# Optimization experiments

Measured on AMD Instinct MI355X. Metric: run time of the kernel, lower is better.

The kernel has to match this reference:

```python
import jax, jax.numpy as jnp
import numpy as np

EMB = 1024
HEADS = 16


def setup_inputs() -> dict:
    key = jax.random.key(0)
    ks = jax.random.split(key, 5)
    s = 1.0 / np.sqrt(EMB).astype(np.float32)
    return {
        "x": jax.random.normal(ks[0], (4, 2048, EMB), dtype=jnp.float32),
        "Wq": jax.random.normal(ks[1], (EMB, EMB), dtype=jnp.float32) * s,
        "bq": jnp.zeros((EMB,), dtype=jnp.float32),
        "Wk": jax.random.normal(ks[2], (EMB, EMB), dtype=jnp.float32) * s,
        "bk": jnp.zeros((EMB,), dtype=jnp.float32),
        "Wv": jax.random.normal(ks[3], (EMB, EMB), dtype=jnp.float32) * s,
        "bv": jnp.zeros((EMB,), dtype=jnp.float32),
        "Wo": jax.random.normal(ks[4], (EMB, EMB), dtype=jnp.float32) * s,
        "bo": jnp.zeros((EMB,), dtype=jnp.float32),
    }


def reference(x, Wq, bq, Wk, bk, Wv, bv, Wo, bo):
    b, n, e = x.shape
    h = HEADS
    d = e // h
    # QKV projections, split heads: [b, n, e] -> [b, h, n, d]
    def split_heads(t):
        return t.reshape(b, n, h, d).transpose(0, 2, 1, 3)
    q = split_heads(x @ Wq + bq)
    k = split_heads(x @ Wk + bk)
    v = split_heads(x @ Wv + bv)
    # NOTE: original scales by sqrt(emb_size), not sqrt(head_dim)
    energy = jnp.einsum('bhqd,bhkd->bhqk', q, k)
    att = jax.nn.softmax(energy / jnp.sqrt(jnp.float32(e)), axis=-1)
    # dropout is identity in eval mode
    out = jnp.einsum('bhqk,bhkd->bhqd', att, v)
    out = out.transpose(0, 2, 1, 3).reshape(b, n, e)
    return out @ Wo + bo
```

## Files before the change

### kernel.cpp

```cpp
#include <hip/hip_runtime.h>

#define EMB   1024
#define SEQ   2048
#define BATCH 4
#define HEADS 16
#define HDIM  64
#define MTOT  8192

typedef __bf16 bf16x8 __attribute__((ext_vector_type(8)));
typedef float  fx4    __attribute__((ext_vector_type(4)));

#if __has_builtin(__builtin_amdgcn_exp2f)
#define EXP2(x) __builtin_amdgcn_exp2f(x)
#else
#define EXP2(x) exp2f(x)
#endif

__device__ __forceinline__ unsigned short f2bf(float f) {
    unsigned u = __builtin_bit_cast(unsigned, f);
    u += 0x7fffu + ((u >> 16) & 1u);
    return (unsigned short)(u >> 16);
}
__device__ __forceinline__ unsigned short bfbits(float f) {
    __bf16 h = (__bf16)f;
    return __builtin_bit_cast(unsigned short, h);
}

#define AS1 __attribute__((address_space(1)))
#define AS3 __attribute__((address_space(3)))
__device__ __forceinline__ void glds16(const void* g, void* l) {
    __builtin_amdgcn_global_load_lds((AS1 void*)g, (AS3 void*)l, 16, 0, 0);
}
#define DRAIN_GLDS() __builtin_amdgcn_s_waitcnt(0x0f70)

#define QSCALE 0.0450842137604569f

__global__ __launch_bounds__(256) void cvt_x_kernel(const float* __restrict__ x,
                                                    unsigned short* __restrict__ xb)
{
    const int idx = (blockIdx.x * 256 + threadIdx.x) * 4;
    const float4 v = *(const float4*)(x + idx);
    ushort4 o;
    o.x = f2bf(v.x); o.y = f2bf(v.y); o.z = f2bf(v.z); o.w = f2bf(v.w);
    *(ushort4*)(xb + idx) = o;
}

__global__ __launch_bounds__(256) void cvt_w_kernel(
    const float* __restrict__ w0, const float* __restrict__ w1,
    const float* __restrict__ w2, const float* __restrict__ w3,
    unsigned short* __restrict__ o0, unsigned short* __restrict__ o1,
    unsigned short* __restrict__ o2, unsigned short* __restrict__ o3)
{
    const int z = blockIdx.z;
    const float* W = z == 0 ? w0 : (z == 1 ? w1 : (z == 2 ? w2 : w3));
    unsigned short* O = z == 0 ? o0 : (z == 1 ? o1 : (z == 2 ? o2 : o3));

    __shared__ float Ws[64][65];
    const int t  = threadIdx.x;
    const int k0 = blockIdx.x * 64, n0 = blockIdx.y * 64;
#pragma unroll
    for (int p = 0; p < 4; ++p) {
        const int row = p * 16 + (t >> 4);
        const int col = (t & 15) * 4;
        const float4 v = *(const float4*)(W + (size_t)(k0 + row) * EMB + n0 + col);
        Ws[row][col]     = v.x; Ws[row][col + 1] = v.y;
        Ws[row][col + 2] = v.z; Ws[row][col + 3] = v.w;
    }
    __syncthreads();
    const int nn = t >> 2;
    const int kb = (t & 3) * 16;
#pragma unroll
    for (int q = 0; q < 2; ++q) {
        const int kk = kb + q * 8;
        ushort4 u0, u1;
        u0.x = f2bf(Ws[kk + 0][nn]); u0.y = f2bf(Ws[kk + 1][nn]);
        u0.z = f2bf(Ws[kk + 2][nn]); u0.w = f2bf(Ws[kk + 3][nn]);
        u1.x = f2bf(Ws[kk + 4][nn]); u1.y = f2bf(Ws[kk + 5][nn]);
        u1.z = f2bf(Ws[kk + 6][nn]); u1.w = f2bf(Ws[kk + 7][nn]);
        *(ushort4*)(O + (size_t)(n0 + nn) * EMB + k0 + kk)     = u0;
        *(ushort4*)(O + (size_t)(n0 + nn) * EMB + k0 + kk + 4) = u1;
    }
}

__global__ __launch_bounds__(256) void gemm_bf16_kernel(
    const unsigned short* __restrict__ Ag,
    const unsigned short* __restrict__ B0, const unsigned short* __restrict__ B1,
    const unsigned short* __restrict__ B2,
    const float* __restrict__ bias0, const float* __restrict__ bias1,
    const float* __restrict__ bias2,
    void* out0, void* out1, void* out2, int mode)
{
    const int z = blockIdx.z;
    const unsigned short* __restrict__ Bg = z == 0 ? B0 : (z == 1 ? B1 : B2);
    const float* __restrict__ bias = z == 0 ? bias0 : (z == 1 ? bias1 : bias2);
    void* outp = z == 0 ? out0 : (z == 1 ? out1 : out2);

    __shared__ unsigned short As[128][32];
    __shared__ unsigned short Bs[128][32];

    const int t    = threadIdx.x;
    const int w    = t >> 6;
    const int lane = t & 63;
    const int low4 = lane & 15;
    const int quad = lane >> 4;
    const int m0 = blockIdx.x * 128;
    const int e0 = blockIdx.y * 128;
    const int we = (w & 1) * 64;
    const int wm = (w >> 1) * 64;

    const int srow   = w * 32 + (lane >> 2);
    const int schunk = (lane & 3) ^ ((lane >> 3) & 3);
    const int scol   = schunk * 8;

    const int fchunk = (quad ^ ((low4 >> 1) & 3)) * 8;

    fx4 acc[4][4] = {};

    for (int k0 = 0; k0 < EMB; k0 += 32) {
        __syncthreads();
        glds16(Ag + (size_t)(m0 + srow) * EMB + k0 + scol,      &As[w * 32][0]);
        glds16(Ag + (size_t)(m0 + srow + 16) * EMB + k0 + scol, &As[w * 32 + 16][0]);
        glds16(Bg + (size_t)(e0 + srow) * EMB + k0 + scol,      &Bs[w * 32][0]);
        glds16(Bg + (size_t)(e0 + srow + 16) * EMB + k0 + scol, &Bs[w * 32 + 16][0]);
        DRAIN_GLDS();
        __syncthreads();

        bf16x8 af[4], bfr[4];
#pragma unroll
        for (int i = 0; i < 4; ++i) {
            af[i]  = *(const bf16x8*)&Bs[we + i * 16 + low4][fchunk];
            bfr[i] = *(const bf16x8*)&As[wm + i * 16 + low4][fchunk];
        }
#pragma unroll
        for (int i = 0; i < 4; ++i)
#pragma unroll
            for (int j = 0; j < 4; ++j)
                acc[i][j] = __builtin_amdgcn_mfma_f32_16x16x32_bf16(af[i], bfr[j], acc[i][j], 0, 0, 0);
    }

    fx4 bv[4];
#pragma unroll
    for (int i = 0; i < 4; ++i)
        bv[i] = *(const fx4*)(bias + e0 + we + i * 16 + quad * 4);

    if (mode == 1) {
#pragma unroll
        for (int i = 0; i < 4; ++i)
#pragma unroll
            for (int j = 0; j < 4; ++j) {
                const int m  = m0 + wm + j * 16 + low4;
                const int eb = e0 + we + i * 16 + quad * 4;
                fx4 o4;
#pragma unroll
                for (int rr = 0; rr < 4; ++rr) o4[rr] = acc[i][j][rr] + bv[i][rr];
                *(fx4*)((float*)outp + (size_t)m * EMB + eb) = o4;
            }
    } else if (z <= 1) {
        const float sc = (z == 0) ? QSCALE : 1.0f;
        unsigned short* o = (unsigned short*)outp;
#pragma unroll
        for (int i = 0; i < 4; ++i)
#pragma unroll
            for (int j = 0; j < 4; ++j) {
                const int m  = m0 + wm + j * 16 + low4;
                const int eb = e0 + we + i * 16 + quad * 4;
                const int bb = m >> 11, n = m & (SEQ - 1);
                const int hh = eb >> 6, db = eb & 63;
                ushort4 o4;
                o4.x = f2bf((acc[i][j][0] + bv[i][0]) * sc);
                o4.y = f2bf((acc[i][j][1] + bv[i][1]) * sc);
                o4.z = f2bf((acc[i][j][2] + bv[i][2]) * sc);
                o4.w = f2bf((acc[i][j][3] + bv[i][3]) * sc);
                *(ushort4*)(o + (((size_t)(bb * HEADS + hh)) * SEQ + n) * HDIM + db) = o4;
            }
    } else {
        unsigned short* o = (unsigned short*)outp;
        const int mbase = m0 + wm;
        const int bb    = mbase >> 11;
        const int nb    = mbase & (SEQ - 1);
#pragma unroll
        for (int i = 0; i < 4; ++i) {
            const int eb = e0 + we + i * 16 + quad * 4;
            const int hh = eb >> 6, db = eb & 63;
#pragma unroll
            for (int rr = 0; rr < 4; ++rr) {
                ushort4 o4;
                o4.x = f2bf(acc[i][0][rr] + bv[i][rr]);
                o4.y = f2bf(acc[i][1][rr] + bv[i][rr]);
                o4.z = f2bf(acc[i][2][rr] + bv[i][rr]);
                o4.w = f2bf(acc[i][3][rr] + bv[i][rr]);
                *(ushort4*)(o + (((size_t)(bb * HEADS + hh)) * HDIM + db + rr) * SEQ
                              + nb + low4 * 4) = o4;
            }
        }
    }
}

__global__ __launch_bounds__(256, 2) void attn_mfma4_kernel(
    const unsigned short* __restrict__ qg, const unsigned short* __restrict__ kg,
    const unsigned short* __restrict__ vg, unsigned short* __restrict__ attb)
{
    __shared__ unsigned short Ks[2][64][64];
    __shared__ unsigned short Vs[2][64][64];
    __shared__ unsigned short Ps[4][4][16][72];

    const int t    = threadIdx.x;
    const int w    = t >> 6;
    const int lane = t & 63;
    const int low4 = lane & 15;
    const int quad = lane >> 4;
    const int q0   = blockIdx.x * 256 + w * 64;
    const int bh   = blockIdx.y;
    const size_t base = (size_t)bh * SEQ * HDIM;

    const int srow8  = lane >> 3;
    const int schunk = (lane & 7) ^ srow8;

    bf16x8 aq[4][2];
#pragma unroll
    for (int s = 0; s < 4; ++s) {
        const size_t qrow = base + (size_t)(q0 + s * 16 + low4) * HDIM;
        aq[s][0] = *(const bf16x8*)(qg + qrow + quad * 8);
        aq[s][1] = *(const bf16x8*)(qg + qrow + 32 + quad * 8);
    }

    fx4 o_acc[4][4] = {};
    float l_i[4][4] = {};
    const fx4 fzero = {0.f, 0.f, 0.f, 0.f};

    {
        const unsigned short* kp = kg + base + (size_t)(w * 16 + srow8) * HDIM + schunk * 8;
        glds16(kp,              &Ks[0][w * 16][0]);
        glds16(kp + 8 * HDIM,   &Ks[0][w * 16 + 8][0]);
        const unsigned short* vp = vg + base + (size_t)(w * 16 + srow8) * SEQ + schunk * 8;
        glds16(vp,              &Vs[0][w * 16][0]);
        glds16(vp + 8 * SEQ,    &Vs[0][w * 16 + 8][0]);
    }

    for (int tt0 = 0; tt0 < SEQ / 64; ++tt0) {
        const int buf = tt0 & 1;
        DRAIN_GLDS();
        __syncthreads();

        bf16x8 kf[4][2], vf[4][2];
#pragma unroll
        for (int tk = 0; tk < 4; ++tk) {
            const int row = tk * 16 + low4;
            const int x7  = low4 & 7;
#pragma unroll
            for (int c = 0; c < 2; ++c) {
                const int lc = (c * 4 + quad) ^ x7;
                kf[tk][c] = *(const bf16x8*)&Ks[buf][row][lc * 8];
                vf[tk][c] = *(const bf16x8*)&Vs[buf][row][lc * 8];
            }
        }

        if (tt0 + 1 < SEQ / 64) {
            const int kv1 = (tt0 + 1) * 64;
            const unsigned short* kp = kg + base + (size_t)(kv1 + w * 16 + srow8) * HDIM + schunk * 8;
            glds16(kp,            &Ks[buf ^ 1][w * 16][0]);
            glds16(kp + 8 * HDIM, &Ks[buf ^ 1][w * 16 + 8][0]);
            const unsigned short* vp = vg + base + (size_t)(w * 16 + srow8) * SEQ + kv1 + schunk * 8;
            glds16(vp,            &Vs[buf ^ 1][w * 16][0]);
            glds16(vp + 8 * SEQ,  &Vs[buf ^ 1][w * 16 + 8][0]);
        }

#pragma unroll
        for (int s = 0; s < 4; ++s) {
            fx4 sa[4];
#pragma unroll
            for (int tk = 0; tk < 4; ++tk) {
                sa[tk] = __builtin_amdgcn_mfma_f32_16x16x32_bf16(aq[s][0], kf[tk][0], fzero, 0, 0, 0);
                sa[tk] = __builtin_amdgcn_mfma_f32_16x16x32_bf16(aq[s][1], kf[tk][1], sa[tk], 0, 0, 0);
            }
#pragma unroll
            for (int r = 0; r < 4; ++r) {
                const float p0 = EXP2(sa[0][r]);
                const float p1 = EXP2(sa[1][r]);
                const float p2 = EXP2(sa[2][r]);
                const float p3 = EXP2(sa[3][r]);
                l_i[s][r] += (p0 + p1) + (p2 + p3);
                uint2 pk;
                pk.x = (unsigned)bfbits(p0) | ((unsigned)bfbits(p1) << 16);
                pk.y = (unsigned)bfbits(p2) | ((unsigned)bfbits(p3) << 16);
                *(uint2*)&Ps[w][s][quad * 4 + r][low4 * 4] = pk;
            }
            bf16x8 pf0 = *(const bf16x8*)&Ps[w][s][low4][quad * 8];
            bf16x8 pf1 = *(const bf16x8*)&Ps[w][s][low4][32 + quad * 8];
#pragma unroll
            for (int t2 = 0; t2 < 4; ++t2) {
                o_acc[s][t2] = __builtin_amdgcn_mfma_f32_16x16x32_bf16(pf0, vf[t2][0], o_acc[s][t2], 0, 0, 0);
                o_acc[s][t2] = __builtin_amdgcn_mfma_f32_16x16x32_bf16(pf1, vf[t2][1], o_acc[s][t2], 0, 0, 0);
            }
        }
    }

#pragma unroll
    for (int s = 0; s < 4; ++s)
#pragma unroll
        for (int r = 0; r < 4; ++r) {
            float v = l_i[s][r];
            for (int off = 1; off < 16; off <<= 1)
                v += __shfl_xor(v, off, 16);
            l_i[s][r] = 1.0f / v;
        }

    const int bb = bh >> 4, hh = bh & 15;
#pragma unroll
    for (int s = 0; s < 4; ++s)
#pragma unroll
        for (int r = 0; r < 4; ++r) {
            const size_t m = (size_t)bb * SEQ + q0 + s * 16 + quad * 4 + r;
#pragma unroll
            for (int t2 = 0; t2 < 4; ++t2) {
                const int e = hh * HDIM + t2 * 16 + low4;
                attb[m * EMB + e] = bfbits(o_acc[s][t2][r] * l_i[s][r]);
            }
        }
}

extern "C" void kernel_launch(void* const* d_in, const int* in_sizes, int n_in,
                              void* d_out, int out_size, void* d_ws, size_t ws_size,
                              hipStream_t stream)
{
    const float* x  = (const float*)d_in[0];
    const float* Wq = (const float*)d_in[1];
    const float* bq = (const float*)d_in[2];
    const float* Wk = (const float*)d_in[3];
    const float* bk = (const float*)d_in[4];
    const float* Wv = (const float*)d_in[5];
    const float* bv = (const float*)d_in[6];
    const float* Wo = (const float*)d_in[7];
    const float* bo = (const float*)d_in[8];

    unsigned short* ws  = (unsigned short*)d_ws;
    unsigned short* xb  = ws;
    unsigned short* wqt = xb + 8388608;
    unsigned short* wkt = wqt + 1048576;
    unsigned short* wvt = wkt + 1048576;
    unsigned short* wot = wvt + 1048576;
    unsigned short* qb  = wot + 1048576;
    unsigned short* kbuf = qb + 8388608;
    unsigned short* vtb  = kbuf + 8388608;
    unsigned short* attb = vtb + 8388608;

    cvt_x_kernel<<<8192, 256, 0, stream>>>(x, xb);
    cvt_w_kernel<<<dim3(16, 16, 4), 256, 0, stream>>>(Wq, Wk, Wv, Wo, wqt, wkt, wvt, wot);

    gemm_bf16_kernel<<<dim3(64, 8, 3), 256, 0, stream>>>(
        xb, wqt, wkt, wvt, bq, bk, bv, qb, kbuf, vtb, 0);

    attn_mfma4_kernel<<<dim3(8, 64), 256, 0, stream>>>(qb, kbuf, vtb, attb);

    gemm_bf16_kernel<<<dim3(64, 8, 1), 256, 0, stream>>>(
        attb, wot, wot, wot, bo, bo, bo, d_out, d_out, d_out, 1);
}
```

Baseline: 282.6 us.

## Compute transposed scores to keep P in registers, removing LDS round-trip

The attention kernel swaps MFMA operand order so it computes S^T = K·Q^T. A permuted K-row mapping makes each lane's exp'd scores line up directly with the B-operand layout needed for the P·V MFMA. This drops the per-wave Ps shared-memory staging buffer, its stores and reloads, and the row-sum shuffle across 16 lanes, which shrinks to two cross-quad shuffles. The output write also becomes vectorised ushort4 stores. It relies on the register layout permutation being exactly correct and changes bf16 rounding of P from manual bit ops to a cast.

After: 271.0 us. -4.1%, faster.

```diff
diff --git a/kernel.cpp b/kernel.cpp
--- a/kernel.cpp
+++ b/kernel.cpp
@@ -196,13 +196,12 @@
     }
 }
 
-__global__ __launch_bounds__(256, 2) void attn_mfma4_kernel(
+__global__ __launch_bounds__(256, 2) void attn_mfma5_kernel(
     const unsigned short* __restrict__ qg, const unsigned short* __restrict__ kg,
     const unsigned short* __restrict__ vg, unsigned short* __restrict__ attb)
 {
     __shared__ unsigned short Ks[2][64][64];
     __shared__ unsigned short Vs[2][64][64];
-    __shared__ unsigned short Ps[4][4][16][72];
 
     const int t    = threadIdx.x;
     const int w    = t >> 6;
@@ -216,6 +215,10 @@
     const int srow8  = lane >> 3;
     const int schunk = (lane & 7) ^ srow8;
 
+    const int tr  = 2 * (low4 >> 2) + (low4 & 1) + 8 * ((low4 >> 1) & 1);
+    const int x7k = tr & 7;
+    const int x7v = low4 & 7;
+
     bf16x8 aq[4][2];
 #pragma unroll
     for (int s = 0; s < 4; ++s) {
@@ -225,7 +228,7 @@
     }
 
     fx4 o_acc[4][4] = {};
-    float l_i[4][4] = {};
+    float l_part[4] = {};
     const fx4 fzero = {0.f, 0.f, 0.f, 0.f};
 
     {
@@ -245,13 +248,10 @@
         bf16x8 kf[4][2], vf[4][2];
 #pragma unroll
         for (int tk = 0; tk < 4; ++tk) {
-            const int row = tk * 16 + low4;
-            const int x7  = low4 & 7;
 #pragma unroll
             for (int c = 0; c < 2; ++c) {
-                const int lc = (c * 4 + quad) ^ x7;
-                kf[tk][c] = *(const bf16x8*)&Ks[buf][row][lc * 8];
-                vf[tk][c] = *(const bf16x8*)&Vs[buf][row][lc * 8];
+                kf[tk][c] = *(const bf16x8*)&Ks[buf][tk * 16 + tr][(((c * 4 + quad) ^ x7k)) * 8];
+                vf[tk][c] = *(const bf16x8*)&Vs[buf][tk * 16 + low4][(((c * 4 + quad) ^ x7v)) * 8];
             }
         }
 
@@ -270,53 +270,60 @@
             fx4 sa[4];
 #pragma unroll
             for (int tk = 0; tk < 4; ++tk) {
-                sa[tk] = __builtin_amdgcn_mfma_f32_16x16x32_bf16(aq[s][0], kf[tk][0], fzero, 0, 0, 0);
-                sa[tk] = __builtin_amdgcn_mfma_f32_16x16x32_bf16(aq[s][1], kf[tk][1], sa[tk], 0, 0, 0);
-            }
-#pragma unroll
-            for (int r = 0; r < 4; ++r) {
-                const float p0 = EXP2(sa[0][r]);
-                const float p1 = EXP2(sa[1][r]);
-                const float p2 = EXP2(sa[2][r]);
-                const float p3 = EXP2(sa[3][r]);
-                l_i[s][r] += (p0 + p1) + (p2 + p3);
-                uint2 pk;
-                pk.x = (unsigned)bfbits(p0) | ((unsigned)bfbits(p1) << 16);
-                pk.y = (unsigned)bfbits(p2) | ((unsigned)bfbits(p3) << 16);
-                *(uint2*)&Ps[w][s][quad * 4 + r][low4 * 4] = pk;
-            }
-            bf16x8 pf0 = *(const bf16x8*)&Ps[w][s][low4][quad * 8];
-            bf16x8 pf1 = *(const bf16x8*)&Ps[w][s][low4][32 + quad * 8];
+                sa[tk] = __builtin_amdgcn_mfma_f32_16x16x32_bf16(kf[tk][0], aq[s][0], fzero, 0, 0, 0);
+                sa[tk] = __builtin_amdgcn_mfma_f32_16x16x32_bf16(kf[tk][1], aq[s][1], sa[tk], 0, 0, 0);
+            }
+            float p[4][4];
+#pragma unroll
+            for (int tk = 0; tk < 4; ++tk)
+#pragma unroll
+                for (int r = 0; r < 4; ++r)
+                    p[tk][r] = EXP2(sa[tk][r]);
+
+            l_part[s] += (((p[0][0] + p[0][1]) + (p[0][2] + p[0][3]))
+                        + ((p[1][0] + p[1][1]) + (p[1][2] + p[1][3])))
+                       + (((p[2][0] + p[2][1]) + (p[2][2] + p[2][3]))
+                        + ((p[3][0] + p[3][1]) + (p[3][2] + p[3][3])));
+
+            bf16x8 pf0, pf1;
+#pragma unroll
+            for (int tk = 0; tk < 4; ++tk) {
+                pf0[tk]     = (__bf16)p[tk][0];
+                pf0[4 + tk] = (__bf16)p[tk][1];
+                pf1[tk]     = (__bf16)p[tk][2];
+                pf1[4 + tk] = (__bf16)p[tk][3];
+            }
 #pragma unroll
             for (int t2 = 0; t2 < 4; ++t2) {
-                o_acc[s][t2] = __builtin_amdgcn_mfma_f32_16x16x32_bf16(pf0, vf[t2][0], o_acc[s][t2], 0, 0, 0);
-                o_acc[s][t2] = __builtin_amdgcn_mfma_f32_16x16x32_bf16(pf1, vf[t2][1], o_acc[s][t2], 0, 0, 0);
-            }
-        }
-    }
-
-#pragma unroll
-    for (int s = 0; s < 4; ++s)
-#pragma unroll
-        for (int r = 0; r < 4; ++r) {
-            float v = l_i[s][r];
-            for (int off = 1; off < 16; off <<= 1)
-                v += __shfl_xor(v, off, 16);
-            l_i[s][r] = 1.0f / v;
-        }
+                o_acc[s][t2] = __builtin_amdgcn_mfma_f32_16x16x32_bf16(vf[t2][0], pf0, o_acc[s][t2], 0, 0, 0);
+                o_acc[s][t2] = __builtin_amdgcn_mfma_f32_16x16x32_bf16(vf[t2][1], pf1, o_acc[s][t2], 0, 0, 0);
+            }
+        }
+    }
+
+    float linv[4];
+#pragma unroll
+    for (int s = 0; s < 4; ++s) {
+        float v = l_part[s];
+        v += __shfl_xor(v, 16);
+        v += __shfl_xor(v, 32);
+        linv[s] = 1.0f / v;
+    }
 
     const int bb = bh >> 4, hh = bh & 15;
 #pragma unroll
-    for (int s = 0; s < 4; ++s)
-#pragma unroll
-        for (int r = 0; r < 4; ++r) {
-            const size_t m = (size_t)bb * SEQ + q0 + s * 16 + quad * 4 + r;
-#pragma unroll
-            for (int t2 = 0; t2 < 4; ++t2) {
-                const int e = hh * HDIM + t2 * 16 + low4;
-                attb[m * EMB + e] = bfbits(o_acc[s][t2][r] * l_i[s][r]);
-            }
-        }
+    for (int s = 0; s < 4; ++s) {
+        const size_t m = (size_t)bb * SEQ + q0 + s * 16 + low4;
+#pragma unroll
+        for (int t2 = 0; t2 < 4; ++t2) {
+            ushort4 o4;
+            o4.x = bfbits(o_acc[s][t2][0] * linv[s]);
+            o4.y = bfbits(o_acc[s][t2][1] * linv[s]);
+            o4.z = bfbits(o_acc[s][t2][2] * linv[s]);
+            o4.w = bfbits(o_acc[s][t2][3] * linv[s]);
+            *(ushort4*)(attb + m * EMB + hh * HDIM + t2 * 16 + quad * 4) = o4;
+        }
+    }
 }
 
 extern "C" void kernel_launch(void* const* d_in, const int* in_sizes, int n_in,
@@ -350,7 +357,7 @@
     gemm_bf16_kernel<<<dim3(64, 8, 3), 256, 0, stream>>>(
         xb, wqt, wkt, wvt, bq, bk, bv, qb, kbuf, vtb, 0);
 
-    attn_mfma4_kernel<<<dim3(8, 64), 256, 0, stream>>>(qb, kbuf, vtb, attb);
+    attn_mfma5_kernel<<<dim3(8, 64), 256, 0, stream>>>(qb, kbuf, vtb, attb);
 
     gemm_bf16_kernel<<<dim3(64, 8, 1), 256, 0, stream>>>(
         attb, wot, wot, wot, bo, bo, bo, d_out, d_out, d_out, 1);
```
